# Optimization experiments

Hardware: AMD Instinct MI355X
Metric: run time of the kernel (lower is better)

## Reference

```python
import jax, jax.numpy as jnp
import numpy as np

N_QUBITS = 10
N_LAYERS = 4
DIM = 2 ** N_QUBITS  # 1024
IN_FEATURES = 512
OUT_FEATURES = 64
BATCH = 4096


def setup_inputs() -> dict:
    key = jax.random.key(0)
    ks = jax.random.split(key, 6)
    return {
        "x": jax.random.normal(ks[0], (BATCH, IN_FEATURES), dtype=jnp.float32),
        "W_pre": jax.random.normal(ks[1], (DIM, IN_FEATURES), dtype=jnp.float32) / np.float32(np.sqrt(IN_FEATURES)),
        "b_pre": jnp.zeros((DIM,), dtype=jnp.float32),
        "q_weights": jax.random.normal(ks[2], (N_LAYERS, N_QUBITS, 3), dtype=jnp.float32),
        "W_post": jax.random.normal(ks[3], (OUT_FEATURES, N_QUBITS), dtype=jnp.float32) / np.float32(np.sqrt(N_QUBITS)),
        "b_post": jnp.zeros((OUT_FEATURES,), dtype=jnp.float32),
    }


def _rot_matrices(w):
    # w: [L, n, 3] -> PennyLane Rot(phi, theta, omega) = RZ(omega) RY(theta) RZ(phi)
    phi, theta, omega = w[..., 0], w[..., 1], w[..., 2]
    c = jnp.cos(theta / 2).astype(jnp.complex64)
    s = jnp.sin(theta / 2).astype(jnp.complex64)
    e_mm = jnp.exp(-0.5j * (phi + omega))
    e_pp = jnp.exp(0.5j * (phi + omega))
    e_pm = jnp.exp(0.5j * (phi - omega))
    e_mp = jnp.exp(-0.5j * (phi - omega))
    row0 = jnp.stack([e_mm * c, -e_pm * s], axis=-1)
    row1 = jnp.stack([e_mp * s, e_pp * c], axis=-1)
    return jnp.stack([row0, row1], axis=-2)  # [L, n, 2, 2] complex64


def _apply_1q(psi, U, wire):
    # psi: [B, 2, 2, ..., 2]; apply 2x2 unitary U on qubit `wire` (axis wire+1)
    axis = wire + 1
    psi = jnp.moveaxis(psi, axis, -1)
    psi = psi @ U.T  # new[a] = sum_b U[a,b] psi[b]
    return jnp.moveaxis(psi, -1, axis)


def _cnot(psi, control, target):
    ca, ta = control + 1, target + 1
    p0 = jax.lax.index_in_dim(psi, 0, ca, keepdims=True)
    p1 = jax.lax.index_in_dim(psi, 1, ca, keepdims=True)
    p1 = jnp.flip(p1, axis=ta)  # flip target amplitudes where control = 1
    return jnp.concatenate([p0, p1], axis=ca)


def _quantum_forward(amps, q_weights):
    # AmplitudeEmbedding(normalize=True) + StronglyEntanglingLayers + PauliZ expvals, batched.
    B = amps.shape[0]
    norm = jnp.sqrt(jnp.sum(amps * amps, axis=1, keepdims=True))
    psi = (amps / norm).astype(jnp.complex64).reshape((B,) + (2,) * N_QUBITS)
    U = _rot_matrices(q_weights)
    for l in range(N_LAYERS):
        for w in range(N_QUBITS):
            psi = _apply_1q(psi, U[l, w], w)
        r = (l % (N_QUBITS - 1)) + 1  # PennyLane default ranges
        for w in range(N_QUBITS):
            psi = _cnot(psi, w, (w + r) % N_QUBITS)
    probs = psi.real ** 2 + psi.imag ** 2
    axes_all = tuple(range(1, N_QUBITS + 1))
    z = []
    for i in range(N_QUBITS):
        other = tuple(a for a in axes_all if a != i + 1)
        marg = jnp.sum(probs, axis=other)  # [B, 2]
        z.append(marg[:, 0] - marg[:, 1])
    return jnp.stack(z, axis=1)  # [B, n_qubits]


def reference(x, W_pre, b_pre, q_weights, W_post, b_post):
    h = jax.nn.relu(x @ W_pre.T + b_pre)          # [B, 2^n]
    z = _quantum_forward(h, q_weights)            # [B, n_qubits]
    return z @ W_post.T + b_post                  # [B, out_features]
```

## Files before the change

kernel.cpp:

```cpp
#include <hip/hip_runtime.h>
#include <hip/hip_bf16.h>
#include <math.h>

#define NQ   10
#define DIM  1024
#define NL   4
#define INF  512
#define OUTF 64
#define MBATCH 4096

typedef _Float16 half8 __attribute__((ext_vector_type(8)));
typedef float f32x4 __attribute__((ext_vector_type(4)));
typedef float f32x2 __attribute__((ext_vector_type(2)));

#define WS_H16  0
#define WS_X16  (8u * 1024u * 1024u)
#define WS_W16  (12u * 1024u * 1024u)
#define WS_SU   (13u * 1024u * 1024u)

constexpr int fstep(int j, int r) {
    for (int w2 = NQ - 1; w2 >= 0; --w2) {
        const int cb = 9 - w2;
        const int tb = 9 - ((w2 + r) % NQ);
        j ^= ((j >> cb) & 1) << tb;
    }
    return j;
}
constexpr int ifstep(int j, int r) {
    for (int w2 = 0; w2 < NQ; ++w2) {
        const int cb = 9 - w2;
        const int tb = 9 - ((w2 + r) % NQ);
        j ^= ((j >> cb) & 1) << tb;
    }
    return j;
}
constexpr int sigma_fwd(int l, int x) {
    for (int t = l - 1; t >= 0; --t) x = fstep(x, t + 1);
    return x;
}
constexpr int sigma_inv(int l, int s) {
    for (int t = 0; t < l; ++t) s = ifstep(s, t + 1);
    return s;
}
constexpr int gate_m(int l, int b) { return sigma_fwd(l, 1 << b); }
constexpr int gate_g(int l, int b) {
    int g = 0;
    for (int j = 0; j < NQ; ++j)
        if ((sigma_inv(l, 1 << j) >> b) & 1) g |= 1 << j;
    return g;
}
struct QM { int v[NQ]; };
constexpr QM make_qm() {
    QM q{};
    for (int w = 0; w < NQ; ++w) {
        const int B = 9 - w;
        int m = 0;
        for (int j = 0; j < NQ; ++j)
            if ((sigma_inv(NL, 1 << j) >> B) & 1) m |= 1 << j;
        q.v[w] = m;
    }
    return q;
}
constexpr QM QMASKS = make_qm();

constexpr int mask_at(int t) { return gate_m(t / 10, 9 - (t % 10)); }
constexpr int pick_wbit() {
    int best = 9, bc = 1000;
    for (int j = 3; j <= 9; ++j) {
        int c = 0;
        for (int t = 0; t < 40; ++t) c += (mask_at(t) >> j) & 1;
        if (c < bc) { bc = c; best = j; }
    }
    return best;
}
constexpr int WBIT = pick_wbit();
struct LP { int v[6]; };
constexpr LP make_lpos() {
    LP p{}; int n = 0;
    for (int j = 3; j <= 9; ++j) if (j != WBIT) p.v[n++] = j;
    return p;
}
constexpr LP LPOS = make_lpos();
constexpr int lx_extract(int m) {
    int r = 0;
    for (int t = 0; t < 6; ++t) if ((m >> LPOS.v[t]) & 1) r |= 1 << t;
    return r;
}

__global__ __launch_bounds__(256) void setup_kernel(
    const float* __restrict__ x, const float* __restrict__ w,
    const float* __restrict__ qw, _Float16* __restrict__ x16,
    _Float16* __restrict__ w16, float* __restrict__ su)
{
    const int bid = blockIdx.x;
    const int tid = threadIdx.x;
    if (bid < 1024) {
        const int base = bid * 2048 + tid * 8;
        float4 a = *reinterpret_cast<const float4*>(x + base);
        float4 b = *reinterpret_cast<const float4*>(x + base + 4);
        half8 o = {(_Float16)a.x, (_Float16)a.y, (_Float16)a.z, (_Float16)a.w,
                   (_Float16)b.x, (_Float16)b.y, (_Float16)b.z, (_Float16)b.w};
        *reinterpret_cast<half8*>(x16 + base) = o;
    } else if (bid < 1280) {
        const int base = (bid - 1024) * 2048 + tid * 8;
        float4 a = *reinterpret_cast<const float4*>(w + base);
        float4 b = *reinterpret_cast<const float4*>(w + base + 4);
        half8 o = {(_Float16)a.x, (_Float16)a.y, (_Float16)a.z, (_Float16)a.w,
                   (_Float16)b.x, (_Float16)b.y, (_Float16)b.z, (_Float16)b.w};
        *reinterpret_cast<half8*>(w16 + base) = o;
    } else {
        if (tid < NL * NQ) {
            float phi = qw[tid * 3 + 0], theta = qw[tid * 3 + 1], omega = qw[tid * 3 + 2];
            float st, ct; sincosf(0.5f * theta, &st, &ct);
            float spm, cpm; sincosf(0.5f * (phi - omega), &spm, &cpm);
            float spp, cpp; sincosf(0.5f * (phi + omega), &spp, &cpp);
            float* o = su + tid * 8;
            o[0] =  cpp * ct; o[1] = -spp * ct;
            o[2] = -cpm * st; o[3] = -spm * st;
            o[4] =  cpm * st; o[5] = -spm * st;
            o[6] =  cpp * ct; o[7] =  spp * ct;
        }
    }
}

__global__ __launch_bounds__(256) void gemm16_kernel(
    const _Float16* __restrict__ X, const _Float16* __restrict__ W,
    const float* __restrict__ bias, _Float16* __restrict__ H)
{
    constexpr int BM = 128, BN = 64, BK = 32, LDP = BK + 8;
    __shared__ _Float16 As[BM][LDP];
    __shared__ _Float16 Bs[BN][LDP];

    const int tid = threadIdx.x;
    const int wave = tid >> 6, lane = tid & 63;
    const int wm = wave >> 1, wn = wave & 1;
    const int l15 = lane & 15, lk = (lane >> 4) * 8;

    const int arow = tid >> 1, ahalf = tid & 1;
    const int brow = tid & 63, bseg = tid >> 6;

    const _Float16* ag = X + (size_t)(blockIdx.x * BM + arow) * INF + ahalf * 16;
    const _Float16* bg = W + (size_t)(blockIdx.y * BN + brow) * INF + bseg * 8;

    f32x4 acc[4][2] = {};

    for (int k0 = 0; k0 < INF; k0 += BK) {
        half8 av0 = *reinterpret_cast<const half8*>(ag + k0);
        half8 av1 = *reinterpret_cast<const half8*>(ag + k0 + 8);
        half8 bv  = *reinterpret_cast<const half8*>(bg + k0);
        __syncthreads();
        *reinterpret_cast<half8*>(&As[arow][ahalf * 16])     = av0;
        *reinterpret_cast<half8*>(&As[arow][ahalf * 16 + 8]) = av1;
        *reinterpret_cast<half8*>(&Bs[brow][bseg * 8])       = bv;
        __syncthreads();
        half8 bfr0 = *reinterpret_cast<const half8*>(&Bs[wn * 32 + l15][lk]);
        half8 bfr1 = *reinterpret_cast<const half8*>(&Bs[wn * 32 + 16 + l15][lk]);
#pragma unroll
        for (int mi = 0; mi < 4; ++mi) {
            half8 afr = *reinterpret_cast<const half8*>(&As[wm * 64 + mi * 16 + l15][lk]);
            acc[mi][0] = __builtin_amdgcn_mfma_f32_16x16x32_f16(afr, bfr0, acc[mi][0], 0, 0, 0);
            acc[mi][1] = __builtin_amdgcn_mfma_f32_16x16x32_f16(afr, bfr1, acc[mi][1], 0, 0, 0);
        }
    }

    const int crow0 = blockIdx.x * BM + wm * 64;
    const int ccol0 = blockIdx.y * BN + wn * 32;
#pragma unroll
    for (int ni = 0; ni < 2; ++ni) {
        const int col = ccol0 + ni * 16 + l15;
        const float bb = bias[col];
#pragma unroll
        for (int mi = 0; mi < 4; ++mi) {
#pragma unroll
            for (int r = 0; r < 4; ++r) {
                const int row = crow0 + mi * 16 + (lane >> 4) * 4 + r;
                const float o = fmaxf(acc[mi][ni][r] + bb, 0.f);
                H[(size_t)row * DIM + col] = (_Float16)o;
            }
        }
    }
}

template<int MHI>
__device__ __forceinline__ int lxi(int v, int lane) {
    if constexpr (MHI == 0)
        return v;
    else if constexpr (MHI == 1)
        return __builtin_amdgcn_mov_dpp(v, 0xB1, 0xF, 0xF, false);
    else if constexpr (MHI == 2)
        return __builtin_amdgcn_mov_dpp(v, 0x4E, 0xF, 0xF, false);
    else if constexpr (MHI == 3)
        return __builtin_amdgcn_mov_dpp(v, 0x1B, 0xF, 0xF, false);
    else if constexpr (MHI == 8)
        return __builtin_amdgcn_mov_dpp(v, 0x128, 0xF, 0xF, false);
    else if constexpr (MHI < 32)
        return __builtin_amdgcn_ds_swizzle(v, 0x1F | (MHI << 10));
    else
        return __builtin_amdgcn_ds_bpermute((lane ^ MHI) << 2, v);
}

template<int MHI>
__device__ __forceinline__ float lxf(float v, int lane) {
    return __int_as_float(lxi<MHI>(__float_as_int(v), lane));
}

__device__ __forceinline__ float allred(float v, int lane) {
    v += lxf<1>(v, lane);
    v += lxf<2>(v, lane);
    v += lxf<4>(v, lane);
    v += lxf<8>(v, lane);
    v += lxf<16>(v, lane);
    v += lxf<32>(v, lane);
    return v;
}

template<int L, int W>
__device__ __forceinline__ void apply_gate(f32x2 rr[4], f32x2 ii[4],
                                           const float* __restrict__ su,
                                           int lane, int wave,
                                           f32x4 (*buf)[2][64])
{
    constexpr int b = 9 - W;
    constexpr int m = gate_m(L, b);
    constexpr int g = gate_g(L, b);
    constexpr int MW    = (m >> WBIT) & 1;
    constexpr int MLANE = lx_extract(m);
    constexpr int MREG  = m & 7;
    constexpr int GW    = (g >> WBIT) & 1;
    constexpr int GLANE = lx_extract(g);
    constexpr int GREG  = g & 7;

    const float4 ua = *reinterpret_cast<const float4*>(su + (L * NQ + W) * 8);
    const float4 ub = *reinterpret_cast<const float4*>(su + (L * NQ + W) * 8 + 4);
    int hli = __builtin_popcount(lane & GLANE) & 1;
    if constexpr (GW) hli ^= wave;
    const bool hl = hli != 0;

    const float cmr0 = hl ? ub.z : ua.x, cmi0 = hl ? ub.w : ua.y;
    const float cpr0 = hl ? ub.x : ua.z, cpi0 = hl ? ub.y : ua.w;
    const float cmr1 = hl ? ua.x : ub.z, cmi1 = hl ? ua.y : ub.w;
    const float cpr1 = hl ? ua.z : ub.x, cpi1 = hl ? ua.w : ub.y;

    float pr[8], pi[8];
    if constexpr (MW == 0) {
#pragma unroll
        for (int k = 0; k < 8; ++k) {
            const int kp = k ^ MREG;
            const float vr = (kp & 1) ? rr[kp >> 1].y : rr[kp >> 1].x;
            const float vi = (kp & 1) ? ii[kp >> 1].y : ii[kp >> 1].x;
            pr[k] = lxf<MLANE>(vr, lane);
            pi[k] = lxf<MLANE>(vi, lane);
        }
    } else {
        buf[0][wave][lane] = f32x4{rr[0].x, rr[0].y, rr[1].x, rr[1].y};
        buf[1][wave][lane] = f32x4{rr[2].x, rr[2].y, rr[3].x, rr[3].y};
        buf[2][wave][lane] = f32x4{ii[0].x, ii[0].y, ii[1].x, ii[1].y};
        buf[3][wave][lane] = f32x4{ii[2].x, ii[2].y, ii[3].x, ii[3].y};
        __syncthreads();
        const int pl = lane ^ MLANE;
        const int pw = wave ^ 1;
        const f32x4 R0 = buf[0][pw][pl];
        const f32x4 R1 = buf[1][pw][pl];
        const f32x4 I0 = buf[2][pw][pl];
        const f32x4 I1 = buf[3][pw][pl];
        __syncthreads();
#pragma unroll
        for (int k = 0; k < 8; ++k) {
            const int kp = k ^ MREG;
            pr[k] = (kp & 4) ? R1[kp & 3] : R0[kp & 3];
            pi[k] = (kp & 4) ? I1[kp & 3] : I0[kp & 3];
        }
    }
#pragma unroll
    for (int j = 0; j < 4; ++j) {
        const int k0 = 2 * j, k1 = 2 * j + 1;
        const int h0 = __builtin_popcount(k0 & GREG) & 1;
        const int h1 = __builtin_popcount(k1 & GREG) & 1;
        f32x2 CMR, CMI, CPR, CPI, PR, PI;
        CMR.x = h0 ? cmr1 : cmr0;  CMR.y = h1 ? cmr1 : cmr0;
        CMI.x = h0 ? cmi1 : cmi0;  CMI.y = h1 ? cmi1 : cmi0;
        CPR.x = h0 ? cpr1 : cpr0;  CPR.y = h1 ? cpr1 : cpr0;
        CPI.x = h0 ? cpi1 : cpi0;  CPI.y = h1 ? cpi1 : cpi0;
        PR.x = pr[k0]; PR.y = pr[k1];
        PI.x = pi[k0]; PI.y = pi[k1];
        const f32x2 R = rr[j], I = ii[j];
        rr[j] = R * CMR - I * CMI + PR * CPR - PI * CPI;
        ii[j] = I * CMR + R * CMI + PI * CPR + PR * CPI;
    }
}

template<int L>
__device__ __forceinline__ void apply_layer(f32x2 rr[4], f32x2 ii[4],
                                            const float* __restrict__ su,
                                            int lane, int wave,
                                            f32x4 (*buf)[2][64])
{
    apply_gate<L, 0>(rr, ii, su, lane, wave, buf);
    apply_gate<L, 1>(rr, ii, su, lane, wave, buf);
    apply_gate<L, 2>(rr, ii, su, lane, wave, buf);
    apply_gate<L, 3>(rr, ii, su, lane, wave, buf);
    apply_gate<L, 4>(rr, ii, su, lane, wave, buf);
    apply_gate<L, 5>(rr, ii, su, lane, wave, buf);
    apply_gate<L, 6>(rr, ii, su, lane, wave, buf);
    apply_gate<L, 7>(rr, ii, su, lane, wave, buf);
    apply_gate<L, 8>(rr, ii, su, lane, wave, buf);
    apply_gate<L, 9>(rr, ii, su, lane, wave, buf);
}

__global__ __launch_bounds__(128, 8) void quantum_kernel(
    const _Float16* __restrict__ Hbuf, const float* __restrict__ sug,
    const float* __restrict__ W_post, const float* __restrict__ b_post,
    float* __restrict__ out)
{
    __shared__ f32x4 buf[4][2][64];
    __shared__ float sred[34];

    const int lane = threadIdx.x;
    const int wave = threadIdx.y;
    const int row  = blockIdx.x;

    int pb = wave << WBIT;
#pragma unroll
    for (int t = 0; t < 6; ++t) pb |= ((lane >> t) & 1) << LPOS.v[t];

    const _Float16* hr = Hbuf + (size_t)row * DIM + pb;
    f32x2 rr[4], ii[4];
    {
        half8 h0 = *reinterpret_cast<const half8*>(hr);
#pragma unroll
        for (int j = 0; j < 4; ++j) {
            rr[j].x = (float)h0[2 * j]; rr[j].y = (float)h0[2 * j + 1];
            ii[j] = f32x2{0.f, 0.f};
        }
    }

    f32x2 n2 = f32x2{0.f, 0.f};
#pragma unroll
    for (int j = 0; j < 4; ++j) n2 += rr[j] * rr[j];
    float nw = allred(n2.x + n2.y, lane);
    if (lane == 0) sred[32 + wave] = nw;
    __syncthreads();
    const float inv_nrm = 1.0f / (sred[32] + sred[33]);

    apply_layer<0>(rr, ii, sug, lane, wave, buf);
    apply_layer<1>(rr, ii, sug, lane, wave, buf);
    apply_layer<2>(rr, ii, sug, lane, wave, buf);
    apply_layer<3>(rr, ii, sug, lane, wave, buf);

    f32x2 P[4];
#pragma unroll
    for (int j = 0; j < 4; ++j) P[j] = rr[j] * rr[j] + ii[j] * ii[j];

    float z[NQ];
#pragma unroll
    for (int w = 0; w < NQ; ++w) {
        const int q = QMASKS.v[w];
        const int qw_ = (q >> WBIT) & 1;
        const int qlane = lx_extract(q);
        const int qreg = q & 7;
        float zl = 0.f;
#pragma unroll
        for (int j = 0; j < 4; ++j) {
            const float s0 = (__builtin_popcount((2 * j) & qreg) & 1) ? -1.f : 1.f;
            const float s1 = (__builtin_popcount((2 * j + 1) & qreg) & 1) ? -1.f : 1.f;
            zl += s0 * P[j].x + s1 * P[j].y;
        }
        int neg = __builtin_popcount(lane & qlane) & 1;
        neg ^= (wave & qw_);
        if (neg) zl = -zl;
        z[w] = allred(zl, lane);
    }
    if (lane == 0) {
#pragma unroll
        for (int w = 0; w < NQ; ++w) sred[wave * 16 + w] = z[w];
    }
    __syncthreads();

    if (wave == 0) {
        float o = b_post[lane];
#pragma unroll
        for (int w = 0; w < NQ; ++w)
            o = fmaf((sred[w] + sred[16 + w]) * inv_nrm, W_post[lane * NQ + w], o);
        out[(size_t)row * OUTF + lane] = o;
    }
}

extern "C" void kernel_launch(void* const* d_in, const int* in_sizes, int n_in,
                              void* d_out, int out_size, void* d_ws, size_t ws_size,
                              hipStream_t stream) {
    const float* x      = (const float*)d_in[0];
    const float* W_pre  = (const float*)d_in[1];
    const float* b_pre  = (const float*)d_in[2];
    const float* qw     = (const float*)d_in[3];
    const float* W_post = (const float*)d_in[4];
    const float* b_post = (const float*)d_in[5];
    float* out = (float*)d_out;

    char* ws = (char*)d_ws;
    _Float16* h16 = (_Float16*)(ws + WS_H16);
    _Float16* x16 = (_Float16*)(ws + WS_X16);
    _Float16* w16 = (_Float16*)(ws + WS_W16);
    float*    su  = (float*)   (ws + WS_SU);

    setup_kernel<<<1281, 256, 0, stream>>>(x, W_pre, qw, x16, w16, su);
    dim3 g1(MBATCH / 128, DIM / 64);
    gemm16_kernel<<<g1, 256, 0, stream>>>(x16, w16, b_pre, h16);
    quantum_kernel<<<MBATCH, dim3(64, 2), 0, stream>>>(h16, su, W_post, b_post, out);
}
```

Baseline: 64.86 us.

## Factor Rot gates into real RY plus merged diagonal phase tables

Each Rot gate is split into RZ·RY·RZ. The RZ phases are commuted through the CNOT permutations and merged into per-basis-state diagonal phase tables, which one small setup block precomputes. That leaves only a real 2x2 rotation per gate and cuts per-gate complex multiply work in the quantum kernel. Separately, the fp32-to-fp16 conversion of x and W_pre now happens inside the GEMM's load path instead of a separate setup pass, removing a kernel's worth of memory traffic. The trade-offs are a serial, trig-heavy single-block setup and four extra diagonal table reads per row.

```diff
diff --git a/kernel.cpp b/kernel.cpp
--- a/kernel.cpp
+++ b/kernel.cpp
@@ -14,11 +14,12 @@
 typedef float f32x2 __attribute__((ext_vector_type(2)));
 
 #define WS_H16  0
-#define WS_X16  (8u * 1024u * 1024u)
-#define WS_W16  (12u * 1024u * 1024u)
-#define WS_SU   (13u * 1024u * 1024u)
-
-constexpr int fstep(int j, int r) {
+#define WS_ROT  (8u * 1024u * 1024u)
+#define WS_TAB  (8u * 1024u * 1024u + 4096u)
+
+#define HD __host__ __device__
+
+HD constexpr int fstep(int j, int r) {
     for (int w2 = NQ - 1; w2 >= 0; --w2) {
         const int cb = 9 - w2;
         const int tb = 9 - ((w2 + r) % NQ);
@@ -26,7 +27,7 @@
     }
     return j;
 }
-constexpr int ifstep(int j, int r) {
+HD constexpr int ifstep(int j, int r) {
     for (int w2 = 0; w2 < NQ; ++w2) {
         const int cb = 9 - w2;
         const int tb = 9 - ((w2 + r) % NQ);
@@ -34,11 +35,11 @@
     }
     return j;
 }
-constexpr int sigma_fwd(int l, int x) {
+HD constexpr int sigma_fwd(int l, int x) {
     for (int t = l - 1; t >= 0; --t) x = fstep(x, t + 1);
     return x;
 }
-constexpr int sigma_inv(int l, int s) {
+HD constexpr int sigma_inv(int l, int s) {
     for (int t = 0; t < l; ++t) s = ifstep(s, t + 1);
     return s;
 }
@@ -88,43 +89,37 @@
 }
 
 __global__ __launch_bounds__(256) void setup_kernel(
-    const float* __restrict__ x, const float* __restrict__ w,
-    const float* __restrict__ qw, _Float16* __restrict__ x16,
-    _Float16* __restrict__ w16, float* __restrict__ su)
-{
-    const int bid = blockIdx.x;
+    const float* __restrict__ qw, float2* __restrict__ rot,
+    float2* __restrict__ tabs)
+{
     const int tid = threadIdx.x;
-    if (bid < 1024) {
-        const int base = bid * 2048 + tid * 8;
-        float4 a = *reinterpret_cast<const float4*>(x + base);
-        float4 b = *reinterpret_cast<const float4*>(x + base + 4);
-        half8 o = {(_Float16)a.x, (_Float16)a.y, (_Float16)a.z, (_Float16)a.w,
-                   (_Float16)b.x, (_Float16)b.y, (_Float16)b.z, (_Float16)b.w};
-        *reinterpret_cast<half8*>(x16 + base) = o;
-    } else if (bid < 1280) {
-        const int base = (bid - 1024) * 2048 + tid * 8;
-        float4 a = *reinterpret_cast<const float4*>(w + base);
-        float4 b = *reinterpret_cast<const float4*>(w + base + 4);
-        half8 o = {(_Float16)a.x, (_Float16)a.y, (_Float16)a.z, (_Float16)a.w,
-                   (_Float16)b.x, (_Float16)b.y, (_Float16)b.z, (_Float16)b.w};
-        *reinterpret_cast<half8*>(w16 + base) = o;
-    } else {
-        if (tid < NL * NQ) {
-            float phi = qw[tid * 3 + 0], theta = qw[tid * 3 + 1], omega = qw[tid * 3 + 2];
-            float st, ct; sincosf(0.5f * theta, &st, &ct);
-            float spm, cpm; sincosf(0.5f * (phi - omega), &spm, &cpm);
-            float spp, cpp; sincosf(0.5f * (phi + omega), &spp, &cpp);
-            float* o = su + tid * 8;
-            o[0] =  cpp * ct; o[1] = -spp * ct;
-            o[2] = -cpm * st; o[3] = -spm * st;
-            o[4] =  cpm * st; o[5] = -spm * st;
-            o[6] =  cpp * ct; o[7] =  spp * ct;
-        }
-    }
-}
-
-__global__ __launch_bounds__(256) void gemm16_kernel(
-    const _Float16* __restrict__ X, const _Float16* __restrict__ W,
+    if (tid < NL * NQ) {
+        float s, c; sincosf(0.5f * qw[tid * 3 + 1], &s, &c);
+        rot[tid] = float2{c, s};
+    }
+    for (int u = 0; u < 4; ++u) {
+        const int s_ = (tid << 2) + u;
+        float a = 0.f;
+        for (int w = 0; w < NQ; ++w)
+            a += qw[w * 3 + 0] * (((s_ >> (9 - w)) & 1) ? 1.f : -1.f);
+        float si, co; sincosf(0.5f * a, &si, &co);
+        tabs[s_] = float2{co, si};
+        for (int l = 0; l < 3; ++l) {
+            const int j  = sigma_inv(l, s_);
+            const int ip = sigma_inv(l + 1, s_);
+            float b = 0.f;
+            for (int w = 0; w < NQ; ++w) {
+                b += qw[(l * NQ + w) * 3 + 2]       * (((j  >> (9 - w)) & 1) ? 1.f : -1.f);
+                b += qw[((l + 1) * NQ + w) * 3 + 0] * (((ip >> (9 - w)) & 1) ? 1.f : -1.f);
+            }
+            sincosf(0.5f * b, &si, &co);
+            tabs[(l + 1) * DIM + s_] = float2{co, si};
+        }
+    }
+}
+
+__global__ __launch_bounds__(256) void gemm_kernel(
+    const float* __restrict__ X, const float* __restrict__ W,
     const float* __restrict__ bias, _Float16* __restrict__ H)
 {
     constexpr int BM = 128, BN = 64, BK = 32, LDP = BK + 8;
@@ -139,19 +134,28 @@
     const int arow = tid >> 1, ahalf = tid & 1;
     const int brow = tid & 63, bseg = tid >> 6;
 
-    const _Float16* ag = X + (size_t)(blockIdx.x * BM + arow) * INF + ahalf * 16;
-    const _Float16* bg = W + (size_t)(blockIdx.y * BN + brow) * INF + bseg * 8;
+    const float* ag = X + (size_t)(blockIdx.x * BM + arow) * INF + ahalf * 16;
+    const float* bg = W + (size_t)(blockIdx.y * BN + brow) * INF + bseg * 8;
 
     f32x4 acc[4][2] = {};
 
     for (int k0 = 0; k0 < INF; k0 += BK) {
-        half8 av0 = *reinterpret_cast<const half8*>(ag + k0);
-        half8 av1 = *reinterpret_cast<const half8*>(ag + k0 + 8);
-        half8 bv  = *reinterpret_cast<const half8*>(bg + k0);
+        float4 a0 = *reinterpret_cast<const float4*>(ag + k0);
+        float4 a1 = *reinterpret_cast<const float4*>(ag + k0 + 4);
+        float4 a2 = *reinterpret_cast<const float4*>(ag + k0 + 8);
+        float4 a3 = *reinterpret_cast<const float4*>(ag + k0 + 12);
+        float4 b0 = *reinterpret_cast<const float4*>(bg + k0);
+        float4 b1 = *reinterpret_cast<const float4*>(bg + k0 + 4);
+        half8 ha0 = {(_Float16)a0.x, (_Float16)a0.y, (_Float16)a0.z, (_Float16)a0.w,
+                     (_Float16)a1.x, (_Float16)a1.y, (_Float16)a1.z, (_Float16)a1.w};
+        half8 ha1 = {(_Float16)a2.x, (_Float16)a2.y, (_Float16)a2.z, (_Float16)a2.w,
+                     (_Float16)a3.x, (_Float16)a3.y, (_Float16)a3.z, (_Float16)a3.w};
+        half8 hb  = {(_Float16)b0.x, (_Float16)b0.y, (_Float16)b0.z, (_Float16)b0.w,
+                     (_Float16)b1.x, (_Float16)b1.y, (_Float16)b1.z, (_Float16)b1.w};
         __syncthreads();
-        *reinterpret_cast<half8*>(&As[arow][ahalf * 16])     = av0;
-        *reinterpret_cast<half8*>(&As[arow][ahalf * 16 + 8]) = av1;
-        *reinterpret_cast<half8*>(&Bs[brow][bseg * 8])       = bv;
+        *reinterpret_cast<half8*>(&As[arow][ahalf * 16])     = ha0;
+        *reinterpret_cast<half8*>(&As[arow][ahalf * 16 + 8]) = ha1;
+        *reinterpret_cast<half8*>(&Bs[brow][bseg * 8])       = hb;
         __syncthreads();
         half8 bfr0 = *reinterpret_cast<const half8*>(&Bs[wn * 32 + l15][lk]);
         half8 bfr1 = *reinterpret_cast<const half8*>(&Bs[wn * 32 + 16 + l15][lk]);
@@ -215,10 +219,10 @@
 }
 
 template<int L, int W>
-__device__ __forceinline__ void apply_gate(f32x2 rr[4], f32x2 ii[4],
-                                           const float* __restrict__ su,
-                                           int lane, int wave,
-                                           f32x4 (*buf)[2][64])
+__device__ __forceinline__ void apply_ry(f32x2 rr[4], f32x2 ii[4],
+                                         const float2* __restrict__ rot,
+                                         int lane, int wave,
+                                         f32x4 (*buf)[2][64])
 {
     constexpr int b = 9 - W;
     constexpr int m = gate_m(L, b);
@@ -230,16 +234,12 @@
     constexpr int GLANE = lx_extract(g);
     constexpr int GREG  = g & 7;
 
-    const float4 ua = *reinterpret_cast<const float4*>(su + (L * NQ + W) * 8);
-    const float4 ub = *reinterpret_cast<const float4*>(su + (L * NQ + W) * 8 + 4);
+    const float2 cs = rot[L * NQ + W];
     int hli = __builtin_popcount(lane & GLANE) & 1;
     if constexpr (GW) hli ^= wave;
-    const bool hl = hli != 0;
-
-    const float cmr0 = hl ? ub.z : ua.x, cmi0 = hl ? ub.w : ua.y;
-    const float cpr0 = hl ? ub.x : ua.z, cpi0 = hl ? ub.y : ua.w;
-    const float cmr1 = hl ? ua.x : ub.z, cmi1 = hl ? ua.y : ub.w;
-    const float cpr1 = hl ? ua.z : ub.x, cpi1 = hl ? ua.w : ub.y;
+    const float sp = hli ? cs.y : -cs.y;
+    const float sn = -sp;
+    const f32x2 C = {cs.x, cs.x};
 
     float pr[8], pi[8];
     if constexpr (MW == 0) {
@@ -274,43 +274,52 @@
 #pragma unroll
     for (int j = 0; j < 4; ++j) {
         const int k0 = 2 * j, k1 = 2 * j + 1;
-        const int h0 = __builtin_popcount(k0 & GREG) & 1;
-        const int h1 = __builtin_popcount(k1 & GREG) & 1;
-        f32x2 CMR, CMI, CPR, CPI, PR, PI;
-        CMR.x = h0 ? cmr1 : cmr0;  CMR.y = h1 ? cmr1 : cmr0;
-        CMI.x = h0 ? cmi1 : cmi0;  CMI.y = h1 ? cmi1 : cmi0;
-        CPR.x = h0 ? cpr1 : cpr0;  CPR.y = h1 ? cpr1 : cpr0;
-        CPI.x = h0 ? cpi1 : cpi0;  CPI.y = h1 ? cpi1 : cpi0;
-        PR.x = pr[k0]; PR.y = pr[k1];
-        PI.x = pi[k0]; PI.y = pi[k1];
+        const float s0 = (__builtin_popcount(k0 & GREG) & 1) ? sn : sp;
+        const float s1 = (__builtin_popcount(k1 & GREG) & 1) ? sn : sp;
+        const f32x2 S = {s0, s1};
+        const f32x2 PR = {pr[k0], pr[k1]};
+        const f32x2 PI = {pi[k0], pi[k1]};
+        rr[j] = C * rr[j] + S * PR;
+        ii[j] = C * ii[j] + S * PI;
+    }
+}
+
+__device__ __forceinline__ void apply_diag(f32x2 rr[4], f32x2 ii[4],
+                                           const f32x4* __restrict__ q)
+{
+#pragma unroll
+    for (int j = 0; j < 4; ++j) {
+        const f32x4 v = q[j];
+        const f32x2 CR = {v.x, v.z};
+        const f32x2 CI = {v.y, v.w};
         const f32x2 R = rr[j], I = ii[j];
-        rr[j] = R * CMR - I * CMI + PR * CPR - PI * CPI;
-        ii[j] = I * CMR + R * CMI + PI * CPR + PR * CPI;
+        rr[j] = R * CR - I * CI;
+        ii[j] = I * CR + R * CI;
     }
 }
 
 template<int L>
 __device__ __forceinline__ void apply_layer(f32x2 rr[4], f32x2 ii[4],
-                                            const float* __restrict__ su,
+                                            const float2* __restrict__ rot,
                                             int lane, int wave,
                                             f32x4 (*buf)[2][64])
 {
-    apply_gate<L, 0>(rr, ii, su, lane, wave, buf);
-    apply_gate<L, 1>(rr, ii, su, lane, wave, buf);
-    apply_gate<L, 2>(rr, ii, su, lane, wave, buf);
-    apply_gate<L, 3>(rr, ii, su, lane, wave, buf);
-    apply_gate<L, 4>(rr, ii, su, lane, wave, buf);
-    apply_gate<L, 5>(rr, ii, su, lane, wave, buf);
-    apply_gate<L, 6>(rr, ii, su, lane, wave, buf);
-    apply_gate<L, 7>(rr, ii, su, lane, wave, buf);
-    apply_gate<L, 8>(rr, ii, su, lane, wave, buf);
-    apply_gate<L, 9>(rr, ii, su, lane, wave, buf);
+    apply_ry<L, 0>(rr, ii, rot, lane, wave, buf);
+    apply_ry<L, 1>(rr, ii, rot, lane, wave, buf);
+    apply_ry<L, 2>(rr, ii, rot, lane, wave, buf);
+    apply_ry<L, 3>(rr, ii, rot, lane, wave, buf);
+    apply_ry<L, 4>(rr, ii, rot, lane, wave, buf);
+    apply_ry<L, 5>(rr, ii, rot, lane, wave, buf);
+    apply_ry<L, 6>(rr, ii, rot, lane, wave, buf);
+    apply_ry<L, 7>(rr, ii, rot, lane, wave, buf);
+    apply_ry<L, 8>(rr, ii, rot, lane, wave, buf);
+    apply_ry<L, 9>(rr, ii, rot, lane, wave, buf);
 }
 
 __global__ __launch_bounds__(128, 8) void quantum_kernel(
-    const _Float16* __restrict__ Hbuf, const float* __restrict__ sug,
-    const float* __restrict__ W_post, const float* __restrict__ b_post,
-    float* __restrict__ out)
+    const _Float16* __restrict__ Hbuf, const float2* __restrict__ rot,
+    const float2* __restrict__ tabs, const float* __restrict__ W_post,
+    const float* __restrict__ b_post, float* __restrict__ out)
 {
     __shared__ f32x4 buf[4][2][64];
     __shared__ float sred[34];
@@ -324,28 +333,40 @@
     for (int t = 0; t < 6; ++t) pb |= ((lane >> t) & 1) << LPOS.v[t];
 
     const _Float16* hr = Hbuf + (size_t)row * DIM + pb;
-    f32x2 rr[4], ii[4];
+    f32x2 A[4];
     {
         half8 h0 = *reinterpret_cast<const half8*>(hr);
 #pragma unroll
-        for (int j = 0; j < 4; ++j) {
-            rr[j].x = (float)h0[2 * j]; rr[j].y = (float)h0[2 * j + 1];
-            ii[j] = f32x2{0.f, 0.f};
-        }
+        for (int j = 0; j < 4; ++j)
+            A[j] = f32x2{(float)h0[2 * j], (float)h0[2 * j + 1]};
     }
 
     f32x2 n2 = f32x2{0.f, 0.f};
 #pragma unroll
-    for (int j = 0; j < 4; ++j) n2 += rr[j] * rr[j];
+    for (int j = 0; j < 4; ++j) n2 += A[j] * A[j];
     float nw = allred(n2.x + n2.y, lane);
     if (lane == 0) sred[32 + wave] = nw;
     __syncthreads();
     const float inv_nrm = 1.0f / (sred[32] + sred[33]);
 
-    apply_layer<0>(rr, ii, sug, lane, wave, buf);
-    apply_layer<1>(rr, ii, sug, lane, wave, buf);
-    apply_layer<2>(rr, ii, sug, lane, wave, buf);
-    apply_layer<3>(rr, ii, sug, lane, wave, buf);
+    f32x2 rr[4], ii[4];
+    {
+        const f32x4* q = reinterpret_cast<const f32x4*>(tabs + pb);
+#pragma unroll
+        for (int j = 0; j < 4; ++j) {
+            const f32x4 v = q[j];
+            rr[j] = A[j] * f32x2{v.x, v.z};
+            ii[j] = A[j] * f32x2{v.y, v.w};
+        }
+    }
+
+    apply_layer<0>(rr, ii, rot, lane, wave, buf);
+    apply_diag(rr, ii, reinterpret_cast<const f32x4*>(tabs + 1 * DIM + pb));
+    apply_layer<1>(rr, ii, rot, lane, wave, buf);
+    apply_diag(rr, ii, reinterpret_cast<const f32x4*>(tabs + 2 * DIM + pb));
+    apply_layer<2>(rr, ii, rot, lane, wave, buf);
+    apply_diag(rr, ii, reinterpret_cast<const f32x4*>(tabs + 3 * DIM + pb));
+    apply_layer<3>(rr, ii, rot, lane, wave, buf);
 
     f32x2 P[4];
 #pragma unroll
@@ -398,12 +419,11 @@
 
     char* ws = (char*)d_ws;
     _Float16* h16 = (_Float16*)(ws + WS_H16);
-    _Float16* x16 = (_Float16*)(ws + WS_X16);
-    _Float16* w16 = (_Float16*)(ws + WS_W16);
-    float*    su  = (float*)   (ws + WS_SU);
-
-    setup_kernel<<<1281, 256, 0, stream>>>(x, W_pre, qw, x16, w16, su);
+    float2*   rot = (float2*)  (ws + WS_ROT);
+    float2*   tabs= (float2*)  (ws + WS_TAB);
+
+    setup_kernel<<<1, 256, 0, stream>>>(qw, rot, tabs);
     dim3 g1(MBATCH / 128, DIM / 64);
-    gemm16_kernel<<<g1, 256, 0, stream>>>(x16, w16, b_pre, h16);
-    quantum_kernel<<<MBATCH, dim3(64, 2), 0, stream>>>(h16, su, W_post, b_post, out);
-}
+    gemm_kernel<<<g1, 256, 0, stream>>>(x, W_pre, b_pre, h16);
+    quantum_kernel<<<MBATCH, dim3(64, 2), 0, stream>>>(h16, rot, tabs, W_post, b_post, out);
+}
```

New measurement: 70.73 us. 1.09x slower.
